# Kernel optimization log

Measured on AMD Instinct MI355X. Metric: run time of the kernel, lower is better.

The kernel has to match this reference:

```python
import jax, jax.numpy as jnp
import numpy as np

EPS = 1e-12  # torch F.normalize eps


def setup_inputs() -> dict:
    key = jax.random.key(0)
    k1, k2, k3, k4, k5 = jax.random.split(key, 5)
    n_drug1 = n_drug2 = 4096
    d = 128
    n_pairs = 1_000_000
    association_pairs = jax.random.randint(k1, (2, n_pairs), 0, n_drug1, dtype=jnp.int64) if jax.config.jax_enable_x64 else jax.random.randint(k1, (2, n_pairs), 0, n_drug1, dtype=jnp.int32)
    drug_embedding1 = jax.random.normal(k2, (n_drug1, d), dtype=jnp.float32)
    drug_embedding2 = jax.random.normal(k3, (n_drug2, d), dtype=jnp.float32)
    W1 = jax.random.normal(k4, (d, n_drug1), dtype=jnp.float32) * (1.0 / np.sqrt(n_drug1))
    W2 = jax.random.normal(k5, (d, n_drug2), dtype=jnp.float32) * (1.0 / np.sqrt(n_drug2))
    return {
        "association_pairs": association_pairs,
        "drug_embedding1": drug_embedding1,
        "drug_embedding2": drug_embedding2,
        "W1": W1,
        "W2": W2,
    }


def reference(association_pairs, drug_embedding1, drug_embedding2, W1, W2):
    # Original does Linear(diag(ones)) which is mathematically W.T; the
    # projected "embedding table" for drug i is column i of W.
    # Gather: table1[idx] == W1[:, idx].T -> [n_pairs, d]
    e1 = jnp.take(W1, association_pairs[0], axis=1).T  # [P, d]
    e2 = jnp.take(W2, association_pairs[1], axis=1).T  # [P, d]
    assoc = e1 * e2                                     # [P, d]
    # F.normalize: x / max(||x||_2, eps) along dim=1
    norm = jnp.linalg.norm(assoc, axis=1, keepdims=True)
    assoc = assoc / jnp.maximum(norm, EPS)
    # dropout in eval mode -> identity
    return assoc
```

## Files before the change

### kernel.cpp

```cpp
#include <hip/hip_runtime.h>
#include <hip/hip_bf16.h>


#define D 128

using f32x4 = __attribute__((ext_vector_type(4))) float;

__global__ __launch_bounds__(256) void transpose_tables(
        const float* __restrict__ W1, const float* __restrict__ W2,
        float* __restrict__ T1, float* __restrict__ T2, int n_drug) {
    __shared__ float tile[32][33];
    const float* W = blockIdx.z ? W2 : W1;
    float*       T = blockIdx.z ? T2 : T1;
    int jt = blockIdx.x * 32;
    int kt = blockIdx.y * 32;
    int tx = threadIdx.x;
    int ty = threadIdx.y;
    #pragma unroll
    for (int r = ty; r < 32; r += 8)
        tile[r][tx] = W[(size_t)(kt + r) * n_drug + jt + tx];
    __syncthreads();
    #pragma unroll
    for (int r = ty; r < 32; r += 8)
        T[(size_t)(jt + r) * D + kt + tx] = tile[tx][r];
}

__global__ __launch_bounds__(256) void gather_mul_normalize(
        const int* __restrict__ pairs,
        const float* __restrict__ T1,
        const float* __restrict__ T2,
        float* __restrict__ out,
        int n_pairs, int n_groups) {
    const int lane  = threadIdx.x & 15;
    const int group = blockIdx.x * (blockDim.x >> 4) + (threadIdx.x >> 4);
    if (group >= n_pairs) return;
    const int last = n_pairs - 1;

    int row = group;
    int i0 = pairs[row];
    int i1 = pairs[n_pairs + row];
    const f32x4* r1 = reinterpret_cast<const f32x4*>(T1 + (size_t)i0 * D);
    const f32x4* r2 = reinterpret_cast<const f32x4*>(T2 + (size_t)i1 * D);
    f32x4 a0 = r1[lane], a1 = r1[lane + 16];
    f32x4 b0 = r2[lane], b1 = r2[lane + 16];

    int nrow   = row + n_groups;
    int nrow_c = nrow <= last ? nrow : last;
    int ni0 = pairs[nrow_c];
    int ni1 = pairs[n_pairs + nrow_c];

    for (;;) {
        int nnrow   = nrow + n_groups;
        int nnrow_c = nnrow <= last ? nnrow : last;
        int nni0 = pairs[nnrow_c];
        int nni1 = pairs[n_pairs + nnrow_c];

        const f32x4* nr1 = reinterpret_cast<const f32x4*>(T1 + (size_t)ni0 * D);
        const f32x4* nr2 = reinterpret_cast<const f32x4*>(T2 + (size_t)ni1 * D);
        f32x4 na0 = nr1[lane], na1 = nr1[lane + 16];
        f32x4 nb0 = nr2[lane], nb1 = nr2[lane + 16];

        f32x4 p0 = a0 * b0;
        f32x4 p1 = a1 * b1;
        float s = p0.x * p0.x + p0.y * p0.y + p0.z * p0.z + p0.w * p0.w
                + p1.x * p1.x + p1.y * p1.y + p1.z * p1.z + p1.w * p1.w;
        #pragma unroll
        for (int m = 8; m >= 1; m >>= 1)
            s += __shfl_xor(s, m);
        float inv = 1.0f / fmaxf(sqrtf(s), 1e-12f);
        p0 *= inv;
        p1 *= inv;
        f32x4* orow = reinterpret_cast<f32x4*>(out + (size_t)row * D);
        __builtin_nontemporal_store(p0, orow + lane);
        __builtin_nontemporal_store(p1, orow + lane + 16);

        if (nrow > last) break;
        row = nrow;
        a0 = na0; a1 = na1; b0 = nb0; b1 = nb1;
        nrow = nnrow; ni0 = nni0; ni1 = nni1;
    }
}

extern "C" void kernel_launch(void* const* d_in, const int* in_sizes, int n_in,
                              void* d_out, int out_size, void* d_ws, size_t ws_size,
                              hipStream_t stream) {
    const int*   pairs = (const int*)d_in[0];
    const float* W1    = (const float*)d_in[3];
    const float* W2    = (const float*)d_in[4];
    float*       out   = (float*)d_out;

    int n_pairs = in_sizes[0] / 2;
    int n_drug  = in_sizes[3] / D;

    float* T1 = (float*)d_ws;
    float* T2 = T1 + (size_t)n_drug * D;

    {
        dim3 grid(n_drug / 32, D / 32, 2);
        dim3 block(32, 8, 1);
        transpose_tables<<<grid, block, 0, stream>>>(W1, W2, T1, T2, n_drug);
    }
    {
        int blocks   = 2048;
        int n_groups = blocks * (256 / 16);
        gather_mul_normalize<<<blocks, 256, 0, stream>>>(pairs, T1, T2, out,
                                                         n_pairs, n_groups);
    }
}
```

Before: 114.6 us.

## Store transposed tables in bf16 and deepen gather prefetch pipeline

The transpose kernel now writes the projected embedding tables as bf16 instead of fp32, which halves the bytes read per gathered row. The gather kernel is also restructured to keep two rows of table data in flight rather than one. The intent is to cut gather bandwidth and hide more latency. In exchange, the product values lose precision (bf16 mantissa), which may exceed the accuracy tolerance, and the deeper pipeline needs more registers.

```diff
diff --git a/kernel.cpp b/kernel.cpp
--- a/kernel.cpp
+++ b/kernel.cpp
@@ -5,13 +5,19 @@
 #define D 128
 
 using f32x4 = __attribute__((ext_vector_type(4))) float;
+using u16x4 = __attribute__((ext_vector_type(4))) unsigned short;
+
+__device__ __forceinline__ float bf2f(unsigned short u) {
+    return __uint_as_float(((unsigned int)u) << 16);
+}
 
 __global__ __launch_bounds__(256) void transpose_tables(
         const float* __restrict__ W1, const float* __restrict__ W2,
-        float* __restrict__ T1, float* __restrict__ T2, int n_drug) {
+        __hip_bfloat16* __restrict__ T1, __hip_bfloat16* __restrict__ T2,
+        int n_drug) {
     __shared__ float tile[32][33];
-    const float* W = blockIdx.z ? W2 : W1;
-    float*       T = blockIdx.z ? T2 : T1;
+    const float*    W = blockIdx.z ? W2 : W1;
+    __hip_bfloat16* T = blockIdx.z ? T2 : T1;
     int jt = blockIdx.x * 32;
     int kt = blockIdx.y * 32;
     int tx = threadIdx.x;
@@ -22,13 +28,25 @@
     __syncthreads();
     #pragma unroll
     for (int r = ty; r < 32; r += 8)
-        T[(size_t)(jt + r) * D + kt + tx] = tile[tx][r];
+        T[(size_t)(jt + r) * D + kt + tx] = __float2bfloat16(tile[tx][r]);
 }
+
+#define LOAD_ROW(dst0, dst1, dst2, dst3, idx0, idx1)                          \
+    {                                                                         \
+        const u16x4* base1 =                                                  \
+            reinterpret_cast<const u16x4*>(T1 + (size_t)(idx0)*D);            \
+        const u16x4* base2 =                                                  \
+            reinterpret_cast<const u16x4*>(T2 + (size_t)(idx1)*D);            \
+        dst0 = base1[lane];                                                   \
+        dst1 = base1[lane + 16];                                              \
+        dst2 = base2[lane];                                                   \
+        dst3 = base2[lane + 16];                                              \
+    }
 
 __global__ __launch_bounds__(256) void gather_mul_normalize(
         const int* __restrict__ pairs,
-        const float* __restrict__ T1,
-        const float* __restrict__ T2,
+        const __hip_bfloat16* __restrict__ T1,
+        const __hip_bfloat16* __restrict__ T2,
         float* __restrict__ out,
         int n_pairs, int n_groups) {
     const int lane  = threadIdx.x & 15;
@@ -39,45 +57,54 @@
     int row = group;
     int i0 = pairs[row];
     int i1 = pairs[n_pairs + row];
-    const f32x4* r1 = reinterpret_cast<const f32x4*>(T1 + (size_t)i0 * D);
-    const f32x4* r2 = reinterpret_cast<const f32x4*>(T2 + (size_t)i1 * D);
-    f32x4 a0 = r1[lane], a1 = r1[lane + 16];
-    f32x4 b0 = r2[lane], b1 = r2[lane + 16];
+    u16x4 a0, a1, b0, b1;
+    LOAD_ROW(a0, a1, b0, b1, i0, i1);
 
-    int nrow   = row + n_groups;
-    int nrow_c = nrow <= last ? nrow : last;
-    int ni0 = pairs[nrow_c];
-    int ni1 = pairs[n_pairs + nrow_c];
+    int r1 = row + n_groups;
+    int r1c = r1 <= last ? r1 : last;
+    int j0 = pairs[r1c];
+    int j1 = pairs[n_pairs + r1c];
+    u16x4 c0, c1, d0, d1;
+    LOAD_ROW(c0, c1, d0, d1, j0, j1);
+
+    int r2 = r1 + n_groups;
+    int r2c = r2 <= last ? r2 : last;
+    int k0 = pairs[r2c];
+    int k1 = pairs[n_pairs + r2c];
 
     for (;;) {
-        int nnrow   = nrow + n_groups;
-        int nnrow_c = nnrow <= last ? nnrow : last;
-        int nni0 = pairs[nnrow_c];
-        int nni1 = pairs[n_pairs + nnrow_c];
+        u16x4 e0, e1, f0, f1;
+        LOAD_ROW(e0, e1, f0, f1, k0, k1);
 
-        const f32x4* nr1 = reinterpret_cast<const f32x4*>(T1 + (size_t)ni0 * D);
-        const f32x4* nr2 = reinterpret_cast<const f32x4*>(T2 + (size_t)ni1 * D);
-        f32x4 na0 = nr1[lane], na1 = nr1[lane + 16];
-        f32x4 nb0 = nr2[lane], nb1 = nr2[lane + 16];
+        int r3  = r2 + n_groups;
+        int r3c = r3 <= last ? r3 : last;
+        int l0 = pairs[r3c];
+        int l1 = pairs[n_pairs + r3c];
 
-        f32x4 p0 = a0 * b0;
-        f32x4 p1 = a1 * b1;
-        float s = p0.x * p0.x + p0.y * p0.y + p0.z * p0.z + p0.w * p0.w
-                + p1.x * p1.x + p1.y * p1.y + p1.z * p1.z + p1.w * p1.w;
+        float p[8];
         #pragma unroll
-        for (int m = 8; m >= 1; m >>= 1)
-            s += __shfl_xor(s, m);
+        for (int q = 0; q < 4; ++q) {
+            p[q]     = bf2f(a0[q]) * bf2f(b0[q]);
+            p[q + 4] = bf2f(a1[q]) * bf2f(b1[q]);
+        }
+        float s = 0.f;
+        #pragma unroll
+        for (int q = 0; q < 8; ++q) s += p[q] * p[q];
+        #pragma unroll
+        for (int m = 8; m >= 1; m >>= 1) s += __shfl_xor(s, m);
         float inv = 1.0f / fmaxf(sqrtf(s), 1e-12f);
-        p0 *= inv;
-        p1 *= inv;
+        f32x4 q0 = {p[0] * inv, p[1] * inv, p[2] * inv, p[3] * inv};
+        f32x4 q1 = {p[4] * inv, p[5] * inv, p[6] * inv, p[7] * inv};
         f32x4* orow = reinterpret_cast<f32x4*>(out + (size_t)row * D);
-        __builtin_nontemporal_store(p0, orow + lane);
-        __builtin_nontemporal_store(p1, orow + lane + 16);
+        __builtin_nontemporal_store(q0, orow + lane);
+        __builtin_nontemporal_store(q1, orow + lane + 16);
 
-        if (nrow > last) break;
-        row = nrow;
-        a0 = na0; a1 = na1; b0 = nb0; b1 = nb1;
-        nrow = nnrow; ni0 = nni0; ni1 = nni1;
+        if (r1 > last) break;
+        row = r1;
+        a0 = c0; a1 = c1; b0 = d0; b1 = d1;
+        c0 = e0; c1 = e1; d0 = f0; d1 = f1;
+        r1 = r2; r2 = r3;
+        k0 = l0; k1 = l1;
     }
 }
 
@@ -92,8 +119,8 @@
     int n_pairs = in_sizes[0] / 2;
     int n_drug  = in_sizes[3] / D;
 
-    float* T1 = (float*)d_ws;
-    float* T2 = T1 + (size_t)n_drug * D;
+    __hip_bfloat16* T1 = (__hip_bfloat16*)d_ws;
+    __hip_bfloat16* T2 = T1 + (size_t)n_drug * D;
 
     {
         dim3 grid(n_drug / 32, D / 32, 2);
```

Measured after the change: 108.3 us. 5.5% less time.
